# Kernel tuning notes

Hardware: AMD Instinct MI355X
Metric: run time of the kernel (lower is better)

The kernel has to match this reference:

```python
import jax, jax.numpy as jnp
import numpy as np

LN_EPS = 1e-5


def layer_norm(x, gamma, beta):
    mu = jnp.mean(x, axis=-1, keepdims=True)
    var = jnp.mean(jnp.square(x - mu), axis=-1, keepdims=True)
    return (x - mu) * jax.lax.rsqrt(var + LN_EPS) * gamma + beta


def setup_inputs() -> dict:
    key = jax.random.key(0)
    ks = jax.random.split(key, 4)
    b, t, d, h, r = 4, 2048, 1024, 4096, 32
    x = jax.random.normal(ks[0], (b, t, d), dtype=jnp.float32)
    L = jax.random.normal(ks[1], (d, r), dtype=jnp.float32) * (1.0 / np.sqrt(d))
    W1 = jax.random.normal(ks[2], (d, h), dtype=jnp.float32) * (1.0 / np.sqrt(d))
    W2 = jax.random.normal(ks[3], (h, d), dtype=jnp.float32) * (1.0 / np.sqrt(h))
    return {
        "x": x, "L": L,
        "W1": W1, "b1": jnp.zeros((h,), jnp.float32),
        "W2": W2, "b2": jnp.zeros((d,), jnp.float32),
        "gamma1": jnp.ones((d,), jnp.float32), "beta1": jnp.zeros((d,), jnp.float32),
        "gamma2": jnp.ones((d,), jnp.float32), "beta2": jnp.zeros((d,), jnp.float32),
    }


def reference(x, L, W1, b1, W2, b2, gamma1, beta1, gamma2, beta2):
    d = x.shape[-1]
    # --- GeodesicAttention on norm1(x) ---
    hn = layer_norm(x, gamma1, beta1)  # (b,t,d)
    g = jnp.eye(d, dtype=x.dtype) + L @ L.T  # PSD metric G = I + L L^T, (d,d)
    # dist_sq[b,i,j] = (x_i - x_j)^T G (x_i - x_j)
    #               = q_i + q_j - 2 x_i^T G x_j   (quadratic expansion; avoids (b,t,t,d) diff tensor)
    xg = jnp.einsum('btd,de->bte', hn, g)          # G x, (b,t,d)
    q = jnp.einsum('btd,btd->bt', xg, hn)          # diag quadratic form, (b,t)
    cross = jnp.einsum('bid,bjd->bij', xg, hn)     # x_i^T G x_j, (b,t,t)
    dist_sq = q[:, :, None] + q[:, None, :] - 2.0 * cross
    attn = jax.nn.softmax(-dist_sq, axis=-1)       # (b,t,t)
    x = x + jnp.einsum('bij,bjd->bid', attn, hn)
    # --- MLP on norm2(x) ---
    hm = layer_norm(x, gamma2, beta2)
    hid = jax.nn.gelu(hm @ W1 + b1, approximate=False)
    x = x + hid @ W2 + b2
    return x
```

## Files before the change

kernel.cpp:

```cpp
#include <hip/hip_runtime.h>
#include <cstdint>

typedef float f32x4 __attribute__((ext_vector_type(4)));
typedef __bf16 bf16x8 __attribute__((ext_vector_type(8)));

#define AS1 __attribute__((address_space(1)))
#define AS3 __attribute__((address_space(3)))

__device__ __forceinline__ void gld_lds16(const void* g, void* l) {
    __builtin_amdgcn_global_load_lds((const AS1 void*)g, (AS3 void*)l, 16, 0, 0);
}

__device__ __forceinline__ unsigned short f2bf(float f) {
    unsigned u = __builtin_bit_cast(unsigned, f);
    u = u + 0x7fffu + ((u >> 16) & 1u);
    return (unsigned short)(u >> 16);
}
__device__ __forceinline__ float bf2f(unsigned short h) {
    unsigned u = ((unsigned)h) << 16;
    return __builtin_bit_cast(float, u);
}

__device__ __forceinline__ void bar() {
    asm volatile("" ::: "memory");
    __builtin_amdgcn_s_barrier();
    asm volatile("" ::: "memory");
}

#define WAITVM(n) asm volatile("s_waitcnt vmcnt(" #n ")" ::: "memory")
#define LGKM0     asm volatile("s_waitcnt lgkmcnt(0)" ::: "memory")
#define SCHED0    __builtin_amdgcn_sched_barrier(0)

__device__ __forceinline__ float gelu_f(float t) {
    return 0.5f * t * (1.0f + erff(t * 0.70710678118654752f));
}

template<int MODE, int TRI>
__global__ __launch_bounds__(256, 3) void gemm128(
    const unsigned short* __restrict__ A, long lda, long sAb,
    const unsigned short* __restrict__ B, long ldb, long sBb,
    void* C, long ldc, long sCb,
    const float* add, long ldadd, long sAddb,
    const float* __restrict__ bias, int K)
{
    constexpr int ABUF = 128 * 64;
    constexpr int BUF  = 2 * ABUF;
    __shared__ char sm[3 * BUF];
    const int tid = threadIdx.x, lane = tid & 63, wid = tid >> 6;
    const int wr = wid >> 1, wc = wid & 1;

    const long zb = blockIdx.z;
    const int nwg  = gridDim.x * gridDim.y;
    const int orig = blockIdx.y * gridDim.x + blockIdx.x;
    const int q8 = nwg >> 3, r8 = nwg & 7;
    const int xcd = orig & 7;
    const int wg  = (xcd < r8 ? xcd * (q8 + 1) : r8 * (q8 + 1) + (xcd - r8) * q8) + (orig >> 3);
    int bx, by;
    if constexpr (TRI == 1) {
        int k = 0;
        while (2 * (k + 1) * (k + 1) + (k + 1) <= wg) ++k;
        const int i = wg - (2 * k * k + k);
        const int R = 2 * k;
        if (i < 2 * (R + 1)) { by = R + (i & 1); bx = i >> 1; }
        else                 { by = R + 1;      bx = R + 1;  }
    } else {
        bx = wg % gridDim.x; by = wg / gridDim.x;
    }

    const char* Ab = (const char*)(A + zb * sAb + (long)by * 128 * lda);
    const char* Bb = (const char*)(B + zb * sBb + (long)bx * 128 * ldb);
    const long ldaB = lda * 2, ldbB = ldb * 2;

    const long gsw = (long)(((tid & 3) ^ ((tid >> 3) & 3)) << 4);
    auto stage = [&](int kt, int b) {
#pragma unroll
        for (int i = 0; i < 2; ++i) {
            const int r = i * 64 + (tid >> 2);
            gld_lds16(Ab + (long)r * ldaB + (long)kt * 64 + gsw,
                      sm + b * BUF + i * 4096 + wid * 1024);
            gld_lds16(Bb + (long)r * ldbB + (long)kt * 64 + gsw,
                      sm + b * BUF + ABUF + i * 4096 + wid * 1024);
        }
    };

    f32x4 acc[4][4] = {};
    const int NT = K / 32;
    const int cc = ((lane >> 4) ^ ((lane >> 1) & 3)) << 4;

    stage(0, 0); stage(1, 1);
    WAITVM(4);
    bar();

#pragma unroll 1
    for (int t = 0; t < NT; ++t) {
        const char* bufp = sm + (t % 3) * BUF;
        bf16x8 af[4], bfr[4];
#pragma unroll
        for (int m = 0; m < 4; ++m) {
            const int R = wr * 64 + m * 16 + (lane & 15);
            af[m] = *(const bf16x8*)(bufp + R * 64 + cc);
        }
#pragma unroll
        for (int n = 0; n < 4; ++n) {
            const int R = wc * 64 + n * 16 + (lane & 15);
            bfr[n] = *(const bf16x8*)(bufp + ABUF + R * 64 + cc);
        }
        if (t + 2 < NT) stage(t + 2, (t + 2) % 3);
        LGKM0; SCHED0;
#pragma unroll
        for (int m = 0; m < 4; ++m)
#pragma unroll
            for (int n = 0; n < 4; ++n)
                acc[m][n] = __builtin_amdgcn_mfma_f32_16x16x32_bf16(
                    af[m], bfr[n], acc[m][n], 0, 0, 0);
        if (t + 1 < NT) {
            if (t + 2 < NT) WAITVM(4); else WAITVM(0);
            bar();
        }
    }

    const long row0 = (long)by * 128 + wr * 64 + (lane >> 4) * 4;
    const long col0 = (long)bx * 128 + wc * 64 + (lane & 15);
#pragma unroll
    for (int m = 0; m < 4; ++m)
#pragma unroll
        for (int n = 0; n < 4; ++n)
#pragma unroll
            for (int j = 0; j < 4; ++j) {
                const long r = row0 + m * 16 + j;
                const long c = col0 + n * 16;
                const float v = acc[m][n][j];
                if (MODE == 0) {
                    ((float*)C)[zb * sCb + r * ldc + c] = v;
                } else if (MODE == 1) {
                    ((float*)C)[zb * sCb + r * ldc + c] = v + add[zb * sAddb + r * ldadd + c];
                } else if (MODE == 2) {
                    ((unsigned short*)C)[zb * sCb + r * ldc + c] = f2bf(gelu_f(v + bias[c]));
                } else {
                    ((float*)C)[zb * sCb + r * ldc + c] = v + bias[c] + add[zb * sAddb + r * ldadd + c];
                }
            }
    if constexpr (TRI == 1) {
        if (by != bx) {
#pragma unroll
            for (int m = 0; m < 4; ++m)
#pragma unroll
                for (int n = 0; n < 4; ++n) {
                    float* dst = (float*)C + zb * sCb + (col0 + n * 16) * ldc + (row0 + m * 16);
                    *(float4*)dst = (float4){acc[m][n][0], acc[m][n][1], acc[m][n][2], acc[m][n][3]};
                }
        }
    }
}

template<int MODE>
__global__ __launch_bounds__(256, 2) void gemm256n(
    const unsigned short* __restrict__ A, long lda, long sAb,
    const unsigned short* __restrict__ B, long ldb, long sBb,
    void* C, long ldc, long sCb,
    const float* add, long ldadd, long sAddb,
    const float* __restrict__ bias, int K)
{
    constexpr int ABUF = 256 * 64;
    constexpr int BBUF = 128 * 64;
    constexpr int BUF  = ABUF + BBUF;
    __shared__ char sm[3 * BUF];
    const int tid = threadIdx.x, lane = tid & 63, wid = tid >> 6;
    const int wr = wid >> 1, wc = wid & 1;

    const long zb = blockIdx.z;
    const int nwg  = gridDim.x * gridDim.y;
    const int orig = blockIdx.y * gridDim.x + blockIdx.x;
    const int q8 = nwg >> 3, r8 = nwg & 7;
    const int xcd = orig & 7;
    const int wg  = (xcd < r8 ? xcd * (q8 + 1) : r8 * (q8 + 1) + (xcd - r8) * q8) + (orig >> 3);
    const int bx = wg % gridDim.x, by = wg / gridDim.x;

    const char* Ab = (const char*)(A + zb * sAb + (long)by * 256 * lda);
    const char* Bb = (const char*)(B + zb * sBb + (long)bx * 128 * ldb);
    const long ldaB = lda * 2, ldbB = ldb * 2;

    const long gsw = (long)(((tid & 3) ^ ((tid >> 3) & 3)) << 4);
    auto stage = [&](int kt, int b) {
#pragma unroll
        for (int i = 0; i < 4; ++i) {
            const int r = i * 64 + (tid >> 2);
            gld_lds16(Ab + (long)r * ldaB + (long)kt * 64 + gsw,
                      sm + b * BUF + i * 4096 + wid * 1024);
        }
#pragma unroll
        for (int i = 0; i < 2; ++i) {
            const int r = i * 64 + (tid >> 2);
            gld_lds16(Bb + (long)r * ldbB + (long)kt * 64 + gsw,
                      sm + b * BUF + ABUF + i * 4096 + wid * 1024);
        }
    };

    f32x4 acc[8][4] = {};
    const int NT = K / 32;
    const int cc = ((lane >> 4) ^ ((lane >> 1) & 3)) << 4;

    stage(0, 0); stage(1, 1);
    WAITVM(6);
    bar();

#pragma unroll 1
    for (int t = 0; t < NT; ++t) {
        const char* bufp = sm + (t % 3) * BUF;
        bf16x8 af[8], bfr[4];
#pragma unroll
        for (int m = 0; m < 8; ++m) {
            const int R = wr * 128 + m * 16 + (lane & 15);
            af[m] = *(const bf16x8*)(bufp + R * 64 + cc);
        }
#pragma unroll
        for (int n = 0; n < 4; ++n) {
            const int R = wc * 64 + n * 16 + (lane & 15);
            bfr[n] = *(const bf16x8*)(bufp + ABUF + R * 64 + cc);
        }
        if (t + 2 < NT) stage(t + 2, (t + 2) % 3);
        LGKM0; SCHED0;
#pragma unroll
        for (int m = 0; m < 8; ++m)
#pragma unroll
            for (int n = 0; n < 4; ++n)
                acc[m][n] = __builtin_amdgcn_mfma_f32_16x16x32_bf16(
                    af[m], bfr[n], acc[m][n], 0, 0, 0);
        if (t + 1 < NT) {
            if (t + 2 < NT) WAITVM(6); else WAITVM(0);
            bar();
        }
    }

    const long row0 = (long)by * 256 + wr * 128 + (lane >> 4) * 4;
    const long col0 = (long)bx * 128 + wc * 64 + (lane & 15);
#pragma unroll
    for (int m = 0; m < 8; ++m)
#pragma unroll
        for (int n = 0; n < 4; ++n)
#pragma unroll
            for (int j = 0; j < 4; ++j) {
                const long r = row0 + m * 16 + j;
                const long c = col0 + n * 16;
                const float v = acc[m][n][j];
                if (MODE == 0) {
                    ((float*)C)[zb * sCb + r * ldc + c] = v;
                } else if (MODE == 1) {
                    ((float*)C)[zb * sCb + r * ldc + c] = v + add[zb * sAddb + r * ldadd + c];
                } else if (MODE == 2) {
                    ((unsigned short*)C)[zb * sCb + r * ldc + c] = f2bf(gelu_f(v + bias[c]));
                } else {
                    ((float*)C)[zb * sCb + r * ldc + c] = v + bias[c] + add[zb * sAddb + r * ldadd + c];
                }
            }
}

__global__ __launch_bounds__(256) void ln_kernel(
    const float* __restrict__ x, const float* __restrict__ gamma, const float* __restrict__ beta,
    unsigned short* __restrict__ out, int ldout, float* qout, int pad)
{
    const int tid = threadIdx.x;
    const long row = blockIdx.x;
    float4 v = ((const float4*)(x + row * 1024))[tid];
    float s = v.x + v.y + v.z + v.w;
    float s2 = v.x * v.x + v.y * v.y + v.z * v.z + v.w * v.w;
#pragma unroll
    for (int off = 32; off; off >>= 1) {
        s  += __shfl_down(s, off);
        s2 += __shfl_down(s2, off);
    }
    __shared__ float red[12];
    const int lane = tid & 63, wid = tid >> 6;
    if (lane == 0) { red[wid] = s; red[4 + wid] = s2; }
    __syncthreads();
    s  = red[0] + red[1] + red[2] + red[3];
    s2 = red[4] + red[5] + red[6] + red[7];
    const float mu = s * (1.0f / 1024.0f);
    const float var = s2 * (1.0f / 1024.0f) - mu * mu;
    const float rs = rsqrtf(var + 1e-5f);
    const float4 g = ((const float4*)gamma)[tid];
    const float4 b = ((const float4*)beta)[tid];
    unsigned short o0 = f2bf((v.x - mu) * rs * g.x + b.x);
    unsigned short o1 = f2bf((v.y - mu) * rs * g.y + b.y);
    unsigned short o2 = f2bf((v.z - mu) * rs * g.z + b.z);
    unsigned short o3 = f2bf((v.w - mu) * rs * g.w + b.w);
    ushort4 ov; ov.x = o0; ov.y = o1; ov.z = o2; ov.w = o3;
    ((ushort4*)(out + row * (long)ldout))[tid] = ov;
    if (pad && tid < 32) out[row * (long)ldout + 1056 + tid] = 0;
    if (qout) {
        float y0 = bf2f(o0), y1 = bf2f(o1), y2 = bf2f(o2), y3 = bf2f(o3);
        float sq = y0 * y0 + y1 * y1 + y2 * y2 + y3 * y3;
#pragma unroll
        for (int off = 32; off; off >>= 1) sq += __shfl_down(sq, off);
        if (lane == 0) red[8 + wid] = sq;
        __syncthreads();
        if (tid == 0) qout[row] = red[8] + red[9] + red[10] + red[11];
    }
}

__global__ __launch_bounds__(256) void u_kernel(
    unsigned short* __restrict__ z, const float* __restrict__ L, float* __restrict__ q)
{
    const int tid = threadIdx.x;
    const long row = blockIdx.x;
    __shared__ float hn[1024];
    __shared__ float part[8][32];
    ushort4 uv = ((const ushort4*)(z + row * 1088))[tid];
    hn[tid * 4 + 0] = bf2f(uv.x);
    hn[tid * 4 + 1] = bf2f(uv.y);
    hn[tid * 4 + 2] = bf2f(uv.z);
    hn[tid * 4 + 3] = bf2f(uv.w);
    __syncthreads();
    const int j = tid & 31, grp = tid >> 5;
    float acc = 0.f;
    const float* Lp = L + j;
#pragma unroll 4
    for (int d = grp * 128; d < grp * 128 + 128; ++d)
        acc += hn[d] * Lp[(long)d * 32];
    part[grp][j] = acc;
    __syncthreads();
    if (tid < 32) {
        float u = 0.f;
#pragma unroll
        for (int g2 = 0; g2 < 8; ++g2) u += part[g2][tid];
        unsigned short ub = f2bf(u);
        z[row * 1088 + 1024 + tid] = ub;
        float uf = bf2f(ub);
        part[0][tid] = uf * uf;
    }
    __syncthreads();
    if (tid == 0) {
        float sq = 0.f;
#pragma unroll
        for (int t2 = 0; t2 < 32; ++t2) sq += part[0][t2];
        q[row] += sq;
    }
}

__global__ __launch_bounds__(256) void softmax_kernel(
    float* S, const float* qb)
{
    const int tid = threadIdx.x;
    const long i = blockIdx.x, bl = blockIdx.y;
    float* Sr = S + (bl * 2048 + i) * 2048;
    const float* qr = qb + bl * 2048;
    float l[8];
    float mx = -1e30f;
#pragma unroll
    for (int c2 = 0; c2 < 8; ++c2) {
        const int jj = tid + c2 * 256;
        l[c2] = 2.0f * Sr[jj] - qr[jj];
        mx = fmaxf(mx, l[c2]);
    }
#pragma unroll
    for (int off = 32; off; off >>= 1) mx = fmaxf(mx, __shfl_xor(mx, off));
    __shared__ float red[8];
    const int lane = tid & 63, wid = tid >> 6;
    if (lane == 0) red[wid] = mx;
    __syncthreads();
    mx = fmaxf(fmaxf(red[0], red[1]), fmaxf(red[2], red[3]));
    float sum = 0.f;
#pragma unroll
    for (int c2 = 0; c2 < 8; ++c2) { l[c2] = __expf(l[c2] - mx); sum += l[c2]; }
#pragma unroll
    for (int off = 32; off; off >>= 1) sum += __shfl_xor(sum, off);
    if (lane == 0) red[4 + wid] = sum;
    __syncthreads();
    sum = red[4] + red[5] + red[6] + red[7];
    const float inv = 1.0f / sum;
    unsigned short* Pr = (unsigned short*)S + (bl * 2048 + i) * 4096;
#pragma unroll
    for (int c2 = 0; c2 < 8; ++c2)
        Pr[tid + c2 * 256] = f2bf(l[c2] * inv);
}

__global__ __launch_bounds__(256) void transpose_v_kernel(
    const unsigned short* __restrict__ z, unsigned short* __restrict__ Vt, long sVtb)
{
    __shared__ unsigned short t[32][33];
    const int tid = threadIdx.x;
    const int tx = tid & 31, ty = tid >> 5;
    const long b = blockIdx.z;
    const long k0 = (long)blockIdx.x * 32, n0 = (long)blockIdx.y * 32;
#pragma unroll
    for (int r = 0; r < 32; r += 8)
        t[r + ty][tx] = z[(b * 2048 + k0 + r + ty) * 1088 + n0 + tx];
    __syncthreads();
#pragma unroll
    for (int r = 0; r < 32; r += 8)
        Vt[b * sVtb + (n0 + r + ty) * 2048 + k0 + tx] = t[tx][r + ty];
}

__global__ __launch_bounds__(256) void cast_transpose_kernel(
    const float* __restrict__ W, unsigned short* __restrict__ Wt, int rows, int cols)
{
    __shared__ float t[32][33];
    const int tid = threadIdx.x;
    const int tx = tid & 31, ty = tid >> 5;
    const long r0 = (long)blockIdx.y * 32, c0 = (long)blockIdx.x * 32;
#pragma unroll
    for (int r = 0; r < 32; r += 8)
        t[r + ty][tx] = W[(r0 + r + ty) * (long)cols + c0 + tx];
    __syncthreads();
#pragma unroll
    for (int r = 0; r < 32; r += 8)
        Wt[(c0 + r + ty) * (long)rows + r0 + tx] = f2bf(t[tx][r + ty]);
}

extern "C" void kernel_launch(void* const* d_in, const int* in_sizes, int n_in,
                              void* d_out, int out_size, void* d_ws, size_t ws_size,
                              hipStream_t stream)
{
    const float* x   = (const float*)d_in[0];
    const float* L   = (const float*)d_in[1];
    const float* W1  = (const float*)d_in[2];
    const float* b1  = (const float*)d_in[3];
    const float* W2  = (const float*)d_in[4];
    const float* b2  = (const float*)d_in[5];
    const float* g1  = (const float*)d_in[6];
    const float* be1 = (const float*)d_in[7];
    const float* g2  = (const float*)d_in[8];
    const float* be2 = (const float*)d_in[9];
    float* out = (float*)d_out;
    unsigned short* z = (unsigned short*)d_out;

    char* wsp = (char*)d_ws;
    float* q = (float*)wsp;
    char* pool = wsp + 32768;
    unsigned short* Vt   = (unsigned short*)pool;
    float*          Smat = (float*)(pool + 16777216);
    unsigned short* W1t = (unsigned short*)pool;
    unsigned short* W2t = (unsigned short*)(pool + 8388608);
    unsigned short* hm  = (unsigned short*)(pool + 16777216);
    unsigned short* hid = (unsigned short*)(pool + 33554432);
    const bool fullMLP = ws_size >= (size_t)32768 + 100663296 + 65536;

    ln_kernel<<<8192, 256, 0, stream>>>(x, g1, be1, z, 1088, q, 1);
    u_kernel<<<8192, 256, 0, stream>>>(z, L, q);

    transpose_v_kernel<<<dim3(64, 32, 4), 256, 0, stream>>>(z, Vt, (long)1024 * 2048);
    gemm128<0, 1><<<dim3(136, 1, 4), 256, 0, stream>>>(
        z, 1088, (long)2048 * 1088,
        z, 1088, (long)2048 * 1088,
        Smat, 2048, (long)2048 * 2048,
        nullptr, 0, 0, nullptr, 1088);
    softmax_kernel<<<dim3(2048, 4), 256, 0, stream>>>(Smat, q);
    gemm128<1, 0><<<dim3(8, 16, 4), 256, 0, stream>>>(
        (const unsigned short*)Smat, 4096, (long)2048 * 4096,
        Vt, 2048, (long)1024 * 2048,
        out, 1024, (long)2048 * 1024,
        x, 1024, (long)2048 * 1024,
        nullptr, 2048);

    cast_transpose_kernel<<<dim3(128, 32), 256, 0, stream>>>(W1, W1t, 1024, 4096);
    cast_transpose_kernel<<<dim3(32, 128), 256, 0, stream>>>(W2, W2t, 4096, 1024);
    ln_kernel<<<8192, 256, 0, stream>>>(out, g2, be2, hm, 1024, nullptr, 0);
    if (fullMLP) {
        gemm256n<2><<<dim3(32, 32, 1), 256, 0, stream>>>(
            hm, 1024, 0, W1t, 1024, 0,
            hid, 4096, 0, nullptr, 0, 0, b1, 1024);
        gemm128<3, 0><<<dim3(8, 64, 1), 256, 0, stream>>>(
            hid, 4096, 0, W2t, 4096, 0,
            out, 1024, 0, out, 1024, 0, b2, 4096);
    } else {
        for (int c = 0; c < 2; ++c) {
            const unsigned short* hmc = hm + (size_t)c * 4096 * 1024;
            float* oc = out + (size_t)c * 4096 * 1024;
            gemm256n<2><<<dim3(32, 16, 1), 256, 0, stream>>>(
                hmc, 1024, 0, W1t, 1024, 0,
                hid, 4096, 0, nullptr, 0, 0, b1, 1024);
            gemm128<3, 0><<<dim3(8, 32, 1), 256, 0, stream>>>(
                hid, 4096, 0, W2t, 4096, 0,
                oc, 1024, 0, oc, 1024, 0, b2, 4096);
        }
    }
}
```

Before: 386.2 us.

## Replace shared-tile GEMMs with per-wave private LDS pipeline kernel

Adds gemm_pw, a 512-thread GEMM in which each of the eight waves stages its own 64x64 A and B sub-tiles into a private double-buffered LDS region. This removes workgroup barriers from the K loop. It replaces gemm256n and the non-triangular gemm128 uses (PV product, MLP up and down projections) with a 256x128 block tile at one workgroup per CU. In exchange, tiles are no longer shared across waves, so each A and B row is loaded several times from global memory, and only two buffers are used where there were three.

```diff
diff --git a/kernel.cpp b/kernel.cpp
--- a/kernel.cpp
+++ b/kernel.cpp
@@ -33,6 +33,95 @@
 
 __device__ __forceinline__ float gelu_f(float t) {
     return 0.5f * t * (1.0f + erff(t * 0.70710678118654752f));
+}
+
+template<int MODE>
+__global__ __launch_bounds__(512, 1) void gemm_pw(
+    const unsigned short* __restrict__ A, long lda, long sAb,
+    const unsigned short* __restrict__ B, long ldb, long sBb,
+    void* C, long ldc, long sCb,
+    const float* add, long ldadd, long sAddb,
+    const float* __restrict__ bias, int K)
+{
+    __shared__ char sm[8 * 16384];
+    const int tid = threadIdx.x, lane = tid & 63, wid = tid >> 6;
+    const int wr = wid >> 1, wc = wid & 1;
+
+    const long zb = blockIdx.z;
+    const int nwg  = gridDim.x * gridDim.y;
+    const int orig = blockIdx.y * gridDim.x + blockIdx.x;
+    const int q8 = nwg >> 3, r8 = nwg & 7;
+    const int xcd = orig & 7;
+    const int wg  = (xcd < r8 ? xcd * (q8 + 1) : r8 * (q8 + 1) + (xcd - r8) * q8) + (orig >> 3);
+    const int bx = wg % gridDim.x, by = wg / gridDim.x;
+
+    const char* Ab = (const char*)(A + zb * sAb + ((long)by * 256 + wr * 64) * lda);
+    const char* Bb = (const char*)(B + zb * sBb + ((long)bx * 128 + wc * 64) * ldb);
+    const long ldaB = lda * 2, ldbB = ldb * 2;
+    char* mybuf = sm + wid * 16384;
+
+    const long gsw = (long)(((lane & 3) ^ ((lane >> 3) & 3)) << 4);
+    auto stage = [&](int kt, int b) {
+        char* d = mybuf + b * 8192;
+        const long kb = (long)kt * 64 + gsw;
+#pragma unroll
+        for (int i = 0; i < 4; ++i) {
+            const int r = i * 16 + (lane >> 2);
+            gld_lds16(Ab + (long)r * ldaB + kb, d + i * 1024);
+            gld_lds16(Bb + (long)r * ldbB + kb, d + 4096 + i * 1024);
+        }
+    };
+
+    f32x4 acc[4][4] = {};
+    const int NT = K / 32;
+    const int cc = ((lane >> 4) ^ ((lane >> 1) & 3)) << 4;
+
+    stage(0, 0); stage(1, 1);
+
+#pragma unroll 1
+    for (int t = 0; t < NT; ++t) {
+        if (t + 1 < NT) WAITVM(8); else WAITVM(0);
+        const char* bufp = mybuf + (t & 1) * 8192;
+        bf16x8 af[4], bfr[4];
+#pragma unroll
+        for (int m = 0; m < 4; ++m) {
+            const int R = m * 16 + (lane & 15);
+            af[m] = *(const bf16x8*)(bufp + R * 64 + cc);
+        }
+#pragma unroll
+        for (int n = 0; n < 4; ++n) {
+            const int R = n * 16 + (lane & 15);
+            bfr[n] = *(const bf16x8*)(bufp + 4096 + R * 64 + cc);
+        }
+        LGKM0; SCHED0;
+        if (t + 2 < NT) stage(t + 2, t & 1);
+#pragma unroll
+        for (int m = 0; m < 4; ++m)
+#pragma unroll
+            for (int n = 0; n < 4; ++n)
+                acc[m][n] = __builtin_amdgcn_mfma_f32_16x16x32_bf16(
+                    af[m], bfr[n], acc[m][n], 0, 0, 0);
+    }
+
+    const long row0 = (long)by * 256 + wr * 64 + (lane >> 4) * 4;
+    const long col0 = (long)bx * 128 + wc * 64 + (lane & 15);
+#pragma unroll
+    for (int m = 0; m < 4; ++m)
+#pragma unroll
+        for (int n = 0; n < 4; ++n)
+#pragma unroll
+            for (int j = 0; j < 4; ++j) {
+                const long r = row0 + m * 16 + j;
+                const long c = col0 + n * 16;
+                const float v = acc[m][n][j];
+                if (MODE == 1) {
+                    ((float*)C)[zb * sCb + r * ldc + c] = v + add[zb * sAddb + r * ldadd + c];
+                } else if (MODE == 2) {
+                    ((unsigned short*)C)[zb * sCb + r * ldc + c] = f2bf(gelu_f(v + bias[c]));
+                } else {
+                    ((float*)C)[zb * sCb + r * ldc + c] = v + bias[c] + add[zb * sAddb + r * ldadd + c];
+                }
+            }
 }
 
 template<int MODE, int TRI>
@@ -151,108 +240,6 @@
                 }
         }
     }
-}
-
-template<int MODE>
-__global__ __launch_bounds__(256, 2) void gemm256n(
-    const unsigned short* __restrict__ A, long lda, long sAb,
-    const unsigned short* __restrict__ B, long ldb, long sBb,
-    void* C, long ldc, long sCb,
-    const float* add, long ldadd, long sAddb,
-    const float* __restrict__ bias, int K)
-{
-    constexpr int ABUF = 256 * 64;
-    constexpr int BBUF = 128 * 64;
-    constexpr int BUF  = ABUF + BBUF;
-    __shared__ char sm[3 * BUF];
-    const int tid = threadIdx.x, lane = tid & 63, wid = tid >> 6;
-    const int wr = wid >> 1, wc = wid & 1;
-
-    const long zb = blockIdx.z;
-    const int nwg  = gridDim.x * gridDim.y;
-    const int orig = blockIdx.y * gridDim.x + blockIdx.x;
-    const int q8 = nwg >> 3, r8 = nwg & 7;
-    const int xcd = orig & 7;
-    const int wg  = (xcd < r8 ? xcd * (q8 + 1) : r8 * (q8 + 1) + (xcd - r8) * q8) + (orig >> 3);
-    const int bx = wg % gridDim.x, by = wg / gridDim.x;
-
-    const char* Ab = (const char*)(A + zb * sAb + (long)by * 256 * lda);
-    const char* Bb = (const char*)(B + zb * sBb + (long)bx * 128 * ldb);
-    const long ldaB = lda * 2, ldbB = ldb * 2;
-
-    const long gsw = (long)(((tid & 3) ^ ((tid >> 3) & 3)) << 4);
-    auto stage = [&](int kt, int b) {
-#pragma unroll
-        for (int i = 0; i < 4; ++i) {
-            const int r = i * 64 + (tid >> 2);
-            gld_lds16(Ab + (long)r * ldaB + (long)kt * 64 + gsw,
-                      sm + b * BUF + i * 4096 + wid * 1024);
-        }
-#pragma unroll
-        for (int i = 0; i < 2; ++i) {
-            const int r = i * 64 + (tid >> 2);
-            gld_lds16(Bb + (long)r * ldbB + (long)kt * 64 + gsw,
-                      sm + b * BUF + ABUF + i * 4096 + wid * 1024);
-        }
-    };
-
-    f32x4 acc[8][4] = {};
-    const int NT = K / 32;
-    const int cc = ((lane >> 4) ^ ((lane >> 1) & 3)) << 4;
-
-    stage(0, 0); stage(1, 1);
-    WAITVM(6);
-    bar();
-
-#pragma unroll 1
-    for (int t = 0; t < NT; ++t) {
-        const char* bufp = sm + (t % 3) * BUF;
-        bf16x8 af[8], bfr[4];
-#pragma unroll
-        for (int m = 0; m < 8; ++m) {
-            const int R = wr * 128 + m * 16 + (lane & 15);
-            af[m] = *(const bf16x8*)(bufp + R * 64 + cc);
-        }
-#pragma unroll
-        for (int n = 0; n < 4; ++n) {
-            const int R = wc * 64 + n * 16 + (lane & 15);
-            bfr[n] = *(const bf16x8*)(bufp + ABUF + R * 64 + cc);
-        }
-        if (t + 2 < NT) stage(t + 2, (t + 2) % 3);
-        LGKM0; SCHED0;
-#pragma unroll
-        for (int m = 0; m < 8; ++m)
-#pragma unroll
-            for (int n = 0; n < 4; ++n)
-                acc[m][n] = __builtin_amdgcn_mfma_f32_16x16x32_bf16(
-                    af[m], bfr[n], acc[m][n], 0, 0, 0);
-        if (t + 1 < NT) {
-            if (t + 2 < NT) WAITVM(6); else WAITVM(0);
-            bar();
-        }
-    }
-
-    const long row0 = (long)by * 256 + wr * 128 + (lane >> 4) * 4;
-    const long col0 = (long)bx * 128 + wc * 64 + (lane & 15);
-#pragma unroll
-    for (int m = 0; m < 8; ++m)
-#pragma unroll
-        for (int n = 0; n < 4; ++n)
-#pragma unroll
-            for (int j = 0; j < 4; ++j) {
-                const long r = row0 + m * 16 + j;
-                const long c = col0 + n * 16;
-                const float v = acc[m][n][j];
-                if (MODE == 0) {
-                    ((float*)C)[zb * sCb + r * ldc + c] = v;
-                } else if (MODE == 1) {
-                    ((float*)C)[zb * sCb + r * ldc + c] = v + add[zb * sAddb + r * ldadd + c];
-                } else if (MODE == 2) {
-                    ((unsigned short*)C)[zb * sCb + r * ldc + c] = f2bf(gelu_f(v + bias[c]));
-                } else {
-                    ((float*)C)[zb * sCb + r * ldc + c] = v + bias[c] + add[zb * sAddb + r * ldadd + c];
-                }
-            }
 }
 
 __global__ __launch_bounds__(256) void ln_kernel(
@@ -445,7 +432,7 @@
         Smat, 2048, (long)2048 * 2048,
         nullptr, 0, 0, nullptr, 1088);
     softmax_kernel<<<dim3(2048, 4), 256, 0, stream>>>(Smat, q);
-    gemm128<1, 0><<<dim3(8, 16, 4), 256, 0, stream>>>(
+    gemm_pw<1><<<dim3(8, 8, 4), 512, 0, stream>>>(
         (const unsigned short*)Smat, 4096, (long)2048 * 4096,
         Vt, 2048, (long)1024 * 2048,
         out, 1024, (long)2048 * 1024,
@@ -456,20 +443,20 @@
     cast_transpose_kernel<<<dim3(32, 128), 256, 0, stream>>>(W2, W2t, 4096, 1024);
     ln_kernel<<<8192, 256, 0, stream>>>(out, g2, be2, hm, 1024, nullptr, 0);
     if (fullMLP) {
-        gemm256n<2><<<dim3(32, 32, 1), 256, 0, stream>>>(
+        gemm_pw<2><<<dim3(32, 32, 1), 512, 0, stream>>>(
             hm, 1024, 0, W1t, 1024, 0,
             hid, 4096, 0, nullptr, 0, 0, b1, 1024);
-        gemm128<3, 0><<<dim3(8, 64, 1), 256, 0, stream>>>(
+        gemm_pw<3><<<dim3(8, 32, 1), 512, 0, stream>>>(
             hid, 4096, 0, W2t, 4096, 0,
             out, 1024, 0, out, 1024, 0, b2, 4096);
     } else {
         for (int c = 0; c < 2; ++c) {
             const unsigned short* hmc = hm + (size_t)c * 4096 * 1024;
             float* oc = out + (size_t)c * 4096 * 1024;
-            gemm256n<2><<<dim3(32, 16, 1), 256, 0, stream>>>(
+            gemm_pw<2><<<dim3(32, 16, 1), 512, 0, stream>>>(
                 hmc, 1024, 0, W1t, 1024, 0,
                 hid, 4096, 0, nullptr, 0, 0, b1, 1024);
-            gemm128<3, 0><<<dim3(8, 32, 1), 256, 0, stream>>>(
+            gemm_pw<3><<<dim3(8, 16, 1), 512, 0, stream>>>(
                 hid, 4096, 0, W2t, 4096, 0,
                 oc, 1024, 0, oc, 1024, 0, b2, 4096);
         }
```

New measurement: 509.8 us. 32.0% more time.
